# Kernel optimization log

Measured on AMD Instinct MI355X. Metric: run time of the kernel, lower is better.

The kernel has to match this reference:

```python
import jax, jax.numpy as jnp
import numpy as np

N = 25600          # total nodes
B = 64             # graphs in batch
NPG = N // B       # nodes per graph (400)
K = 16             # in-degree (regular graph)
E = N * K          # edges
D = 128            # hidden dim = out dim
L = 4              # DGN layers
NUM_ATOM = 128


def _linear_init(key, out_s, in_s):
    lim = 1.0 / np.sqrt(in_s)
    return jax.random.uniform(key, (out_s, in_s), jnp.float32, -lim, lim)


def setup_inputs() -> dict:
    key = jax.random.key(0)
    ks = jax.random.split(key, 16)
    node_feat = jax.random.randint(ks[0], (N,), 0, NUM_ATOM)
    # K-regular in-degree graph, edges intra-graph; dst sorted
    dst = jnp.repeat(jnp.arange(N), K)                       # [E]
    src_local = jax.random.randint(ks[1], (E,), 0, NPG)
    src = (dst // NPG) * NPG + src_local                     # same graph as dst
    eig = jax.random.normal(ks[2], (E, 2), jnp.float32)
    snorm_n = jnp.full((N, 1), 1.0 / np.sqrt(NPG), jnp.float32)
    graph_ids = jnp.arange(N) // NPG
    emb = jax.random.normal(ks[3], (NUM_ATOM, D), jnp.float32) * 0.02
    pre_W = jnp.stack([_linear_init(jax.random.fold_in(ks[4], i), D, 2 * D) for i in range(L)])
    pre_b = jnp.zeros((L, D), jnp.float32)
    post_W = jnp.stack([_linear_init(jax.random.fold_in(ks[5], i), D, 5 * D) for i in range(L)])
    post_b = jnp.zeros((L, D), jnp.float32)
    r_W0 = _linear_init(ks[6], 64, 128); r_b0 = jnp.zeros((64,), jnp.float32)
    r_W1 = _linear_init(ks[7], 32, 64);  r_b1 = jnp.zeros((32,), jnp.float32)
    r_W2 = _linear_init(ks[8], 128, 32); r_b2 = jnp.zeros((128,), jnp.float32)
    return dict(node_feat=node_feat, src=src, dst=dst, eig=eig, snorm_n=snorm_n,
                graph_ids=graph_ids, emb=emb, pre_W=pre_W, pre_b=pre_b,
                post_W=post_W, post_b=post_b, r_W0=r_W0, r_b0=r_b0,
                r_W1=r_W1, r_b1=r_b1, r_W2=r_W2, r_b2=r_b2)


def _dgn_layer(h, src, dst, eig, snorm_n, Wp, bp, Wq, bq):
    n = h.shape[0]
    # pretrans on edges: Linear(cat(h_src, h_dst))  [E, D]
    z2 = jnp.concatenate([h[src], h[dst]], axis=-1)
    e = jnp.einsum('ei,oi->eo', z2, Wp) + bp
    seg_sum = lambda v: jax.ops.segment_sum(v, dst, num_segments=n, indices_are_sorted=True)
    s = seg_sum(e)
    mean = s / K
    mx = jax.ops.segment_max(e, dst, num_segments=n, indices_are_sorted=True)
    # directional aggregator (eig_idx=1)
    w = eig[:, 1]
    denom = seg_sum(jnp.abs(w)) + 1e-8                       # [n]
    ew = w / denom[dst]                                      # [E]
    dir_agg = jnp.abs(seg_sum(e * ew[:, None]) - seg_sum(ew)[:, None] * h)
    agg = jnp.concatenate([h, mean, s, mx, dir_agg], axis=-1)  # [n, 5D]
    hn = jnp.einsum('ni,oi->no', agg, Wq) + bq
    hn = hn * snorm_n           # graph_norm
    hn = jax.nn.relu(hn)
    return h + hn               # residual (in_dim == out_dim)


def reference(node_feat, src, dst, eig, snorm_n, graph_ids, emb,
              pre_W, pre_b, post_W, post_b,
              r_W0, r_b0, r_W1, r_b1, r_W2, r_b2):
    h = emb[node_feat]                                       # AtomEncoder
    for i in range(L):
        h = _dgn_layer(h, src, dst, eig, snorm_n, pre_W[i], pre_b[i], post_W[i], post_b[i])
    # mean_nodes per graph (equal-sized graphs)
    hg = jax.ops.segment_sum(h, graph_ids, num_segments=B, indices_are_sorted=True) / NPG
    y = jax.nn.relu(hg @ r_W0.T + r_b0)
    y = jax.nn.relu(y @ r_W1.T + r_b1)
    return y @ r_W2.T + r_b2                                 # [B, 128]
```

## Files before the change

### kernel.cpp

```cpp
#include <hip/hip_runtime.h>
#include <cstddef>

#define NN 25600
#define BB 64
#define NPG 400
#define KK 16
#define LL 4

typedef _Float16 half_t;
typedef _Float16 h8 __attribute__((ext_vector_type(8)));
typedef _Float16 h4 __attribute__((ext_vector_type(4)));
typedef _Float16 h2 __attribute__((ext_vector_type(2)));
typedef float f32x4 __attribute__((ext_vector_type(4)));

__global__ __launch_bounds__(256) void prep_k(const float* __restrict__ preW,
                                              const float* __restrict__ preb,
                                              const float* __restrict__ postW,
                                              half_t* __restrict__ WpreH,
                                              half_t* __restrict__ WpreL,
                                              float* __restrict__ bpre,
                                              half_t* __restrict__ WpostH,
                                              half_t* __restrict__ WpostL) {
  int idx = blockIdx.x * 256 + threadIdx.x;
  const int n1 = LL * 256 * 128;
  const int n2 = n1 + LL * 256;
  const int n3 = n2 + LL * 128 * 512;
  if (idx < n1) {
    int l = idx / 32768;
    int q = idx % 32768;
    int j = q & 7, lane = (q >> 3) & 63, kc = (q >> 9) & 3, c16 = q >> 11;
    int col = c16 * 16 + (lane & 15);
    int k = kc * 32 + (lane >> 4) * 8 + j;
    float v = (col < 128) ? preW[(size_t)l * 32768 + (size_t)col * 256 + k]
                          : preW[(size_t)l * 32768 + (size_t)(col - 128) * 256 + 128 + k];
    half_t hi = (half_t)v;
    WpreH[idx] = hi;
    WpreL[idx] = (half_t)(v - (float)hi);
  } else if (idx < n2) {
    int r = idx - n1;
    int l = r / 256, o = r % 256;
    bpre[r] = (o < 128) ? 0.f : preb[l * 128 + (o - 128)];
  } else if (idx < n3) {
    int r = idx - n2;
    int l = r / 65536;
    int q = r % 65536;
    int j = q & 7, lane = (q >> 3) & 63, kc = (q >> 9) & 15, c16 = q >> 13;
    int col = c16 * 16 + (lane & 15);
    int k = kc * 32 + (lane >> 4) * 8 + j;
    int jblk = k >> 7, kk = k & 127;
    const float* base = postW + (size_t)l * 128 * 640 + (size_t)col * 640;
    float v;
    if (jblk == 0)      v = base[kk];
    else if (jblk == 1) v = base[128 + kk] * (1.f / 16.f) + base[256 + kk];
    else if (jblk == 2) v = base[384 + kk];
    else                v = base[512 + kk];
    half_t hi = (half_t)v;
    WpostH[r] = hi;
    WpostL[r] = (half_t)(v - (float)hi);
  }
}

__global__ __launch_bounds__(256) void embed_k(const int* __restrict__ nf,
                                               const float* __restrict__ emb,
                                               half_t* __restrict__ Hh,
                                               half_t* __restrict__ Hl) {
  int idx = blockIdx.x * 256 + threadIdx.x;
  int n = idx >> 5;
  int d4 = idx & 31;
  int a = nf[n];
  float4 v = *(const float4*)(emb + (size_t)a * 128 + d4 * 4);
  h4 hi, lo;
  const float* vp = &v.x;
#pragma unroll
  for (int j = 0; j < 4; ++j) {
    half_t h = (half_t)vp[j];
    hi[j] = h;
    lo[j] = (half_t)(vp[j] - (float)h);
  }
  *(h4*)(Hh + (size_t)n * 128 + d4 * 4) = hi;
  *(h4*)(Hl + (size_t)n * 128 + d4 * 4) = lo;
}

__global__ __launch_bounds__(256) void pre_gemm_k(const half_t* __restrict__ Ah_g,
                                                  const half_t* __restrict__ Al_g,
                                                  const half_t* __restrict__ Wh_g,
                                                  const half_t* __restrict__ Wl_g,
                                                  float* __restrict__ preA) {
  __shared__ half_t Ahs[64][132];
  __shared__ half_t Als[64][132];
  const int tid = threadIdx.x;
  const int bid = blockIdx.x;
  const int swz = (bid & 7) * 50 + (bid >> 3);
  const int r0 = swz * 64;
  const int wid = tid >> 6, lane = tid & 63;
  const int wm = wid >> 1, wn = wid & 1;
  const int lr = lane & 15, lk = (lane >> 4) * 8;
  f32x4 acc[2][4] = {};

  {
    const int row = tid >> 2;
#pragma unroll
    for (int s = 0; s < 4; ++s) {
      const int koff = (tid & 3) * 8 + s * 32;
      const size_t g = (size_t)(r0 + row) * 128 + koff;
      *(h8*)&Ahs[row][koff] = *(const h8*)(Ah_g + g);
      *(h8*)&Als[row][koff] = *(const h8*)(Al_g + g);
    }
  }
  __syncthreads();

#pragma unroll
  for (int kc = 0; kc < 4; ++kc) {
    h8 af[2][2];
#pragma unroll
    for (int mi = 0; mi < 2; ++mi) {
      const int r = wm * 32 + mi * 16 + lr;
      af[mi][0] = *(const h8*)&Ahs[r][kc * 32 + lk];
      af[mi][1] = *(const h8*)&Als[r][kc * 32 + lk];
    }
#pragma unroll
    for (int nj = 0; nj < 4; ++nj) {
      const size_t fi = ((size_t)((wn * 4 + nj) * 4 + kc) * 64 + lane) * 8;
      const h8 b0v = *(const h8*)(Wh_g + fi);
      const h8 b1v = *(const h8*)(Wl_g + fi);
#pragma unroll
      for (int mi = 0; mi < 2; ++mi) {
        acc[mi][nj] = __builtin_amdgcn_mfma_f32_16x16x32_f16(af[mi][0], b0v, acc[mi][nj], 0, 0, 0);
        acc[mi][nj] = __builtin_amdgcn_mfma_f32_16x16x32_f16(af[mi][0], b1v, acc[mi][nj], 0, 0, 0);
        acc[mi][nj] = __builtin_amdgcn_mfma_f32_16x16x32_f16(af[mi][1], b0v, acc[mi][nj], 0, 0, 0);
      }
    }
  }
#pragma unroll
  for (int mi = 0; mi < 2; ++mi) {
    const int rowb = r0 + wm * 32 + mi * 16 + (lane >> 4) * 4;
#pragma unroll
    for (int nj = 0; nj < 4; ++nj) {
      const int col = wn * 64 + nj * 16 + lr;
#pragma unroll
      for (int q = 0; q < 4; ++q) {
        preA[(size_t)(rowb + q) * 128 + col] = acc[mi][nj][q];
      }
    }
  }
}

__global__ __launch_bounds__(256) void agg_post_k(const float* __restrict__ preA,
                                                  const int* __restrict__ src,
                                                  const float* __restrict__ eig,
                                                  const half_t* __restrict__ WpHg,
                                                  const half_t* __restrict__ WpLg,
                                                  const float* __restrict__ bpre128,
                                                  half_t* __restrict__ Hh,
                                                  half_t* __restrict__ Hl,
                                                  const half_t* __restrict__ Wh,
                                                  const half_t* __restrict__ Wl,
                                                  const float* __restrict__ bias,
                                                  const float* __restrict__ snorm) {
  __shared__ half_t Ah[16][392];
  __shared__ half_t Al[16][392];
  __shared__ float bsh[16][132];
  const int tid = threadIdx.x;
  const int bid = blockIdx.x;
  const int swz = (bid & 7) * 200 + (bid >> 3);
  const int r0 = swz * 16;
  const int wid = tid >> 6, lane = tid & 63;
  const int wn = wid;
  const int lr = lane & 15, lk = (lane >> 4) * 8;
  const int d0 = 2 * lane;

  const int frow = r0 + lr;
  h8 afh[4][2];
#pragma unroll
  for (int hc = 0; hc < 4; ++hc) {
    afh[hc][0] = *(const h8*)(Hh + (size_t)frow * 128 + hc * 32 + lk);
    afh[hc][1] = *(const h8*)(Hl + (size_t)frow * 128 + hc * 32 + lk);
  }

  {
    f32x4 bacc[2] = {};
#pragma unroll
    for (int kc = 0; kc < 4; ++kc) {
#pragma unroll
      for (int nj = 0; nj < 2; ++nj) {
        const size_t fi = ((size_t)((8 + wn * 2 + nj) * 4 + kc) * 64 + lane) * 8;
        const h8 b0v = *(const h8*)(WpHg + fi);
        const h8 b1v = *(const h8*)(WpLg + fi);
        bacc[nj] = __builtin_amdgcn_mfma_f32_16x16x32_f16(afh[kc][0], b0v, bacc[nj], 0, 0, 0);
        bacc[nj] = __builtin_amdgcn_mfma_f32_16x16x32_f16(afh[kc][0], b1v, bacc[nj], 0, 0, 0);
        bacc[nj] = __builtin_amdgcn_mfma_f32_16x16x32_f16(afh[kc][1], b0v, bacc[nj], 0, 0, 0);
      }
    }
    const int rowb = (lane >> 4) * 4;
#pragma unroll
    for (int nj = 0; nj < 2; ++nj) {
      const int col = (wn * 2 + nj) * 16 + lr;
      const float bv = bpre128[col];
#pragma unroll
      for (int q = 0; q < 4; ++q) {
        bsh[rowb + q][col] = bacc[nj][q] + bv;
      }
    }
  }
  __syncthreads();

  for (int i = 0; i < 4; ++i) {
    const int lrow = wid * 4 + i;
    const int n = r0 + lrow;
    int sv[KK];
    float wv[KK];
    {
      const int4* sp4 = (const int4*)(src + (size_t)n * KK);
      const float4* ep4 = (const float4*)(eig + (size_t)n * KK * 2);
#pragma unroll
      for (int t = 0; t < 4; ++t) {
        const int4 s4 = sp4[t];
        sv[4 * t + 0] = s4.x;
        sv[4 * t + 1] = s4.y;
        sv[4 * t + 2] = s4.z;
        sv[4 * t + 3] = s4.w;
      }
#pragma unroll
      for (int t = 0; t < 8; ++t) {
        const float4 e4 = ep4[t];
        wv[2 * t + 0] = e4.y;
        wv[2 * t + 1] = e4.w;
      }
    }
    float denom = 0.f;
#pragma unroll
    for (int e = 0; e < KK; ++e) denom += fabsf(wv[e]);
    denom += 1e-8f;
    const float inv = 1.f / denom;
    float sum_ew = 0.f;
#pragma unroll
    for (int e = 0; e < KK; ++e) {
      wv[e] *= inv;
      sum_ew += wv[e];
    }
    float sA0 = 0.f, sA1 = 0.f, wA0 = 0.f, wA1 = 0.f;
    float mA0 = -3.402823466e+38f, mA1 = -3.402823466e+38f;
#pragma unroll
    for (int e = 0; e < KK; ++e) {
      const float2 a = *(const float2*)(preA + (size_t)sv[e] * 128 + d0);
      sA0 += a.x;
      sA1 += a.y;
      wA0 = fmaf(wv[e], a.x, wA0);
      wA1 = fmaf(wv[e], a.y, wA1);
      mA0 = fmaxf(mA0, a.x);
      mA1 = fmaxf(mA1, a.y);
    }
    const float2 b = {bsh[lrow][d0], bsh[lrow][d0 + 1]};
    const h2 hh2 = *(const h2*)(Hh + (size_t)n * 128 + d0);
    const h2 hl2 = *(const h2*)(Hl + (size_t)n * 128 + d0);
    const float hx = (float)hh2[0] + (float)hl2[0];
    const float hy = (float)hh2[1] + (float)hl2[1];
    auto wr2 = [&](int kcol, float v0, float v1) {
      h2 hi, lo;
      hi[0] = (half_t)v0;
      hi[1] = (half_t)v1;
      lo[0] = (half_t)(v0 - (float)hi[0]);
      lo[1] = (half_t)(v1 - (float)hi[1]);
      *(h2*)&Ah[lrow][kcol] = hi;
      *(h2*)&Al[lrow][kcol] = lo;
    };
    wr2(d0, sA0 + 16.f * b.x, sA1 + 16.f * b.y);
    wr2(128 + d0, mA0 + b.x, mA1 + b.y);
    wr2(256 + d0, fabsf(wA0 + sum_ew * (b.x - hx)), fabsf(wA1 + sum_ew * (b.y - hy)));
  }
  __syncthreads();

  f32x4 acc[2] = {};
#pragma unroll
  for (int kc = 0; kc < 16; ++kc) {
    h8 a0, a1;
    if (kc < 4) {
      a0 = afh[kc & 3][0];
      a1 = afh[kc & 3][1];
    } else {
      a0 = *(const h8*)&Ah[lr][(kc - 4) * 32 + lk];
      a1 = *(const h8*)&Al[lr][(kc - 4) * 32 + lk];
    }
#pragma unroll
    for (int nj = 0; nj < 2; ++nj) {
      const size_t fi = ((size_t)((wn * 2 + nj) * 16 + kc) * 64 + lane) * 8;
      const h8 b0v = *(const h8*)(Wh + fi);
      const h8 b1v = *(const h8*)(Wl + fi);
      acc[nj] = __builtin_amdgcn_mfma_f32_16x16x32_f16(a0, b0v, acc[nj], 0, 0, 0);
      acc[nj] = __builtin_amdgcn_mfma_f32_16x16x32_f16(a0, b1v, acc[nj], 0, 0, 0);
      acc[nj] = __builtin_amdgcn_mfma_f32_16x16x32_f16(a1, b0v, acc[nj], 0, 0, 0);
    }
  }

  const int rowb = r0 + (lane >> 4) * 4;
#pragma unroll
  for (int nj = 0; nj < 2; ++nj) {
    const int col = wn * 32 + nj * 16 + lr;
    const float bv = bias[col];
#pragma unroll
    for (int q = 0; q < 4; ++q) {
      const int r = rowb + q;
      float a = acc[nj][q] + bv;
      a *= snorm[r];
      a = fmaxf(a, 0.f);
      const size_t off = (size_t)r * 128 + col;
      const float hold = (float)Hh[off] + (float)Hl[off];
      const float hn = hold + a;
      const half_t hi = (half_t)hn;
      Hh[off] = hi;
      Hl[off] = (half_t)(hn - (float)hi);
    }
  }
}

__global__ __launch_bounds__(256) void reduce_mlp_k(const half_t* __restrict__ Hh,
                                                    const half_t* __restrict__ Hl,
                                                    const float* __restrict__ W0, const float* __restrict__ b0,
                                                    const float* __restrict__ W1, const float* __restrict__ b1,
                                                    const float* __restrict__ W2, const float* __restrict__ b2,
                                                    float* __restrict__ out) {
  __shared__ float hgs[128];
  __shared__ float red[128];
  __shared__ float y0s[64];
  __shared__ float y1s[32];
  __shared__ float wb[64 * 130];
  const int g = blockIdx.x;
  const int t = threadIdx.x;
  {
    const int d = t & 127, hf = t >> 7;
    const size_t base = ((size_t)g * NPG + (size_t)hf * 200) * 128 + d;
    float acc = 0.f;
    for (int i = 0; i < 200; ++i) {
      const size_t off = base + (size_t)i * 128;
      acc += (float)Hh[off] + (float)Hl[off];
    }
    if (hf) red[d] = acc;
    __syncthreads();
    if (!hf) hgs[d] = (acc + red[d]) * (1.f / (float)NPG);
  }
  __syncthreads();
  for (int idx = t; idx < 64 * 128; idx += 256) {
    wb[(idx >> 7) * 130 + (idx & 127)] = W0[idx];
  }
  __syncthreads();
  if (t < 64) {
    float a = b0[t];
    const float* w = &wb[t * 130];
    for (int k = 0; k < 128; ++k) a = fmaf(hgs[k], w[k], a);
    y0s[t] = fmaxf(a, 0.f);
  }
  __syncthreads();
  for (int idx = t; idx < 32 * 64; idx += 256) {
    wb[(idx >> 6) * 66 + (idx & 63)] = W1[idx];
  }
  __syncthreads();
  if (t < 32) {
    float a = b1[t];
    const float* w = &wb[t * 66];
    for (int k = 0; k < 64; ++k) a = fmaf(y0s[k], w[k], a);
    y1s[t] = fmaxf(a, 0.f);
  }
  __syncthreads();
  for (int idx = t; idx < 128 * 32; idx += 256) {
    wb[(idx >> 5) * 34 + (idx & 31)] = W2[idx];
  }
  __syncthreads();
  if (t < 128) {
    float a = b2[t];
    const float* w = &wb[t * 34];
    for (int k = 0; k < 32; ++k) a = fmaf(y1s[k], w[k], a);
    out[(size_t)g * 128 + t] = a;
  }
}

extern "C" void kernel_launch(void* const* d_in, const int* in_sizes, int n_in,
                              void* d_out, int out_size, void* d_ws, size_t ws_size,
                              hipStream_t stream) {
  const int* node_feat = (const int*)d_in[0];
  const int* src = (const int*)d_in[1];
  const float* eig = (const float*)d_in[3];
  const float* snorm = (const float*)d_in[4];
  const float* emb = (const float*)d_in[6];
  const float* preW = (const float*)d_in[7];
  const float* preb = (const float*)d_in[8];
  const float* postW = (const float*)d_in[9];
  const float* postb = (const float*)d_in[10];
  const float* rW0 = (const float*)d_in[11];
  const float* rb0 = (const float*)d_in[12];
  const float* rW1 = (const float*)d_in[13];
  const float* rb1 = (const float*)d_in[14];
  const float* rW2 = (const float*)d_in[15];
  const float* rb2 = (const float*)d_in[16];
  float* out = (float*)d_out;

  half_t* Hh = (half_t*)d_ws;
  half_t* Hl = Hh + (size_t)NN * 128;
  float* preA = (float*)(Hl + (size_t)NN * 128);
  half_t* WpreH = (half_t*)(preA + (size_t)NN * 128);
  half_t* WpreL = WpreH + (size_t)LL * 32768;
  half_t* WpostH = WpreL + (size_t)LL * 32768;
  half_t* WpostL = WpostH + (size_t)LL * 65536;
  float* bpre = (float*)(WpostL + (size_t)LL * 65536);

  prep_k<<<1540, 256, 0, stream>>>(preW, preb, postW, WpreH, WpreL, bpre, WpostH, WpostL);
  embed_k<<<(NN * 32) / 256, 256, 0, stream>>>(node_feat, emb, Hh, Hl);

  for (int l = 0; l < LL; ++l) {
    pre_gemm_k<<<NN / 64, 256, 0, stream>>>(
        Hh, Hl, WpreH + (size_t)l * 32768, WpreL + (size_t)l * 32768, preA);
    agg_post_k<<<NN / 16, 256, 0, stream>>>(
        preA, src, eig,
        WpreH + (size_t)l * 32768, WpreL + (size_t)l * 32768,
        bpre + (size_t)l * 256 + 128,
        Hh, Hl,
        WpostH + (size_t)l * 65536, WpostL + (size_t)l * 65536,
        postb + (size_t)l * 128, snorm);
  }

  reduce_mlp_k<<<BB, 256, 0, stream>>>(Hh, Hl, rW0, rb0, rW1, rb1, rW2, rb2, out);
}
```

Before: 280.1 us.

## Double the aggregation kernel's wave count and stage neighbor gathers through LDS via async loads

The aggregation/post-GEMM kernel now launches 512 threads (8 waves) per 16-row block, each wave owning one 16-column slice of the MFMA work and two node rows of aggregation instead of four. Neighbor feature rows of preA are brought in with global_load_lds into a per-wave LDS staging buffer, split into 8-edge chunks and interleaved with index/weight loads and reductions behind explicit waitcnt barriers. The aim is more memory-level parallelism and latency hiding for the random gather. In exchange LDS use grows by 32KB per block, which may limit occupancy, and the hand-placed waitcnts are fragile.

```diff
diff --git a/kernel.cpp b/kernel.cpp
--- a/kernel.cpp
+++ b/kernel.cpp
@@ -12,6 +12,9 @@
 typedef _Float16 h4 __attribute__((ext_vector_type(4)));
 typedef _Float16 h2 __attribute__((ext_vector_type(2)));
 typedef float f32x4 __attribute__((ext_vector_type(4)));
+
+#define GCAST(p) ((const __attribute__((address_space(1))) void*)(p))
+#define SCAST(p) ((__attribute__((address_space(3))) void*)(p))
 
 __global__ __launch_bounds__(256) void prep_k(const float* __restrict__ preW,
                                               const float* __restrict__ preb,
@@ -145,21 +148,22 @@
   }
 }
 
-__global__ __launch_bounds__(256) void agg_post_k(const float* __restrict__ preA,
-                                                  const int* __restrict__ src,
-                                                  const float* __restrict__ eig,
-                                                  const half_t* __restrict__ WpHg,
-                                                  const half_t* __restrict__ WpLg,
-                                                  const float* __restrict__ bpre128,
-                                                  half_t* __restrict__ Hh,
-                                                  half_t* __restrict__ Hl,
-                                                  const half_t* __restrict__ Wh,
-                                                  const half_t* __restrict__ Wl,
-                                                  const float* __restrict__ bias,
-                                                  const float* __restrict__ snorm) {
+__global__ __launch_bounds__(512, 4) void agg_post_k(const float* __restrict__ preA,
+                                                     const int* __restrict__ src,
+                                                     const float* __restrict__ eig,
+                                                     const half_t* __restrict__ WpHg,
+                                                     const half_t* __restrict__ WpLg,
+                                                     const float* __restrict__ bpre128,
+                                                     half_t* __restrict__ Hh,
+                                                     half_t* __restrict__ Hl,
+                                                     const half_t* __restrict__ Wh,
+                                                     const half_t* __restrict__ Wl,
+                                                     const float* __restrict__ bias,
+                                                     const float* __restrict__ snorm) {
   __shared__ half_t Ah[16][392];
   __shared__ half_t Al[16][392];
   __shared__ float bsh[16][132];
+  __shared__ float stage[8][8][128];
   const int tid = threadIdx.x;
   const int bid = blockIdx.x;
   const int swz = (bid & 7) * 200 + (bid >> 3);
@@ -168,6 +172,85 @@
   const int wn = wid;
   const int lr = lane & 15, lk = (lane >> 4) * 8;
   const int d0 = 2 * lane;
+  const int glane = (lane & 31) * 4;
+  const int gsel = lane >> 5;
+
+#define LOAD_SE(sv, wv, n)                                              \
+  {                                                                     \
+    const int4* sp4 = (const int4*)(src + (size_t)(n) * KK);            \
+    const float4* ep4 = (const float4*)(eig + (size_t)(n) * KK * 2);    \
+    _Pragma("unroll")                                                   \
+    for (int t = 0; t < 4; ++t) {                                       \
+      const int4 s4 = sp4[t];                                           \
+      sv[4 * t + 0] = s4.x; sv[4 * t + 1] = s4.y;                       \
+      sv[4 * t + 2] = s4.z; sv[4 * t + 3] = s4.w;                       \
+    }                                                                   \
+    _Pragma("unroll")                                                   \
+    for (int t = 0; t < 8; ++t) {                                       \
+      const float4 e4 = ep4[t];                                         \
+      wv[2 * t + 0] = e4.y; wv[2 * t + 1] = e4.w;                       \
+    }                                                                   \
+  }
+#define ISSUE_CHUNK(sv, base)                                                        \
+  {                                                                                  \
+    _Pragma("unroll")                                                                \
+    for (int c = 0; c < 4; ++c) {                                                    \
+      const float* gp = preA + (size_t)sv[(base) + 2 * c + gsel] * 128 + glane;      \
+      __builtin_amdgcn_global_load_lds(GCAST(gp), SCAST(&stage[wid][2 * c][0]),      \
+                                       16, 0, 0);                                    \
+    }                                                                                \
+  }
+#define CONSUME_CHUNK(wv, base, sX, sY, wX, wY, mX, mY)                              \
+  {                                                                                  \
+    _Pragma("unroll")                                                                \
+    for (int e = 0; e < 8; ++e) {                                                    \
+      const float2 a = *(const float2*)&stage[wid][e][d0];                           \
+      const float w = wv[(base) + e];                                                \
+      sX += a.x; sY += a.y;                                                          \
+      wX = fmaf(w, a.x, wX); wY = fmaf(w, a.y, wY);                                  \
+      mX = fmaxf(mX, a.x); mY = fmaxf(mY, a.y);                                      \
+    }                                                                                \
+  }
+#define WEIGHTS(wv, inv, sum_ew)                                                     \
+  {                                                                                  \
+    float denom = 0.f;                                                               \
+    _Pragma("unroll")                                                                \
+    for (int e = 0; e < KK; ++e) denom += fabsf(wv[e]);                              \
+    denom += 1e-8f;                                                                  \
+    inv = 1.f / denom;                                                               \
+    sum_ew = 0.f;                                                                    \
+    _Pragma("unroll")                                                                \
+    for (int e = 0; e < KK; ++e) { wv[e] *= inv; sum_ew += wv[e]; }                  \
+  }
+#define WRITE_ROW(lrow, n, sX, sY, wX, wY, mX, mY, sum_ew)                           \
+  {                                                                                  \
+    const float2 b = {bsh[lrow][d0], bsh[lrow][d0 + 1]};                             \
+    const h2 hh2 = *(const h2*)(Hh + (size_t)(n) * 128 + d0);                        \
+    const h2 hl2 = *(const h2*)(Hl + (size_t)(n) * 128 + d0);                        \
+    const float hx = (float)hh2[0] + (float)hl2[0];                                  \
+    const float hy = (float)hh2[1] + (float)hl2[1];                                  \
+    auto wr2 = [&](int kcol, float v0, float v1) {                                   \
+      h2 hi, lo;                                                                     \
+      hi[0] = (half_t)v0; hi[1] = (half_t)v1;                                        \
+      lo[0] = (half_t)(v0 - (float)hi[0]);                                           \
+      lo[1] = (half_t)(v1 - (float)hi[1]);                                           \
+      *(h2*)&Ah[lrow][kcol] = hi;                                                    \
+      *(h2*)&Al[lrow][kcol] = lo;                                                    \
+    };                                                                               \
+    wr2(d0, sX + 16.f * b.x, sY + 16.f * b.y);                                       \
+    wr2(128 + d0, mX + b.x, mY + b.y);                                               \
+    wr2(256 + d0, fabsf(wX + sum_ew * (b.x - hx)),                                   \
+                  fabsf(wY + sum_ew * (b.y - hy)));                                  \
+  }
+#define LGKM0 asm volatile("s_waitcnt lgkmcnt(0)" ::: "memory");
+#define VM0   asm volatile("s_waitcnt vmcnt(0)" ::: "memory");
+
+  const int lrowA = wid * 2;
+  const int nA = r0 + lrowA;
+  int svA[KK];
+  float wvA[KK];
+  LOAD_SE(svA, wvA, nA)
+  ISSUE_CHUNK(svA, 0)
 
   const int frow = r0 + lr;
   h8 afh[4][2];
@@ -178,99 +261,59 @@
   }
 
   {
-    f32x4 bacc[2] = {};
+    f32x4 bacc = {};
 #pragma unroll
     for (int kc = 0; kc < 4; ++kc) {
-#pragma unroll
-      for (int nj = 0; nj < 2; ++nj) {
-        const size_t fi = ((size_t)((8 + wn * 2 + nj) * 4 + kc) * 64 + lane) * 8;
-        const h8 b0v = *(const h8*)(WpHg + fi);
-        const h8 b1v = *(const h8*)(WpLg + fi);
-        bacc[nj] = __builtin_amdgcn_mfma_f32_16x16x32_f16(afh[kc][0], b0v, bacc[nj], 0, 0, 0);
-        bacc[nj] = __builtin_amdgcn_mfma_f32_16x16x32_f16(afh[kc][0], b1v, bacc[nj], 0, 0, 0);
-        bacc[nj] = __builtin_amdgcn_mfma_f32_16x16x32_f16(afh[kc][1], b0v, bacc[nj], 0, 0, 0);
-      }
+      const size_t fi = ((size_t)((8 + wn) * 4 + kc) * 64 + lane) * 8;
+      const h8 b0v = *(const h8*)(WpHg + fi);
+      const h8 b1v = *(const h8*)(WpLg + fi);
+      bacc = __builtin_amdgcn_mfma_f32_16x16x32_f16(afh[kc][0], b0v, bacc, 0, 0, 0);
+      bacc = __builtin_amdgcn_mfma_f32_16x16x32_f16(afh[kc][0], b1v, bacc, 0, 0, 0);
+      bacc = __builtin_amdgcn_mfma_f32_16x16x32_f16(afh[kc][1], b0v, bacc, 0, 0, 0);
     }
     const int rowb = (lane >> 4) * 4;
-#pragma unroll
-    for (int nj = 0; nj < 2; ++nj) {
-      const int col = (wn * 2 + nj) * 16 + lr;
-      const float bv = bpre128[col];
-#pragma unroll
-      for (int q = 0; q < 4; ++q) {
-        bsh[rowb + q][col] = bacc[nj][q] + bv;
-      }
-    }
-  }
-  __syncthreads();
-
-  for (int i = 0; i < 4; ++i) {
-    const int lrow = wid * 4 + i;
-    const int n = r0 + lrow;
-    int sv[KK];
-    float wv[KK];
-    {
-      const int4* sp4 = (const int4*)(src + (size_t)n * KK);
-      const float4* ep4 = (const float4*)(eig + (size_t)n * KK * 2);
-#pragma unroll
-      for (int t = 0; t < 4; ++t) {
-        const int4 s4 = sp4[t];
-        sv[4 * t + 0] = s4.x;
-        sv[4 * t + 1] = s4.y;
-        sv[4 * t + 2] = s4.z;
-        sv[4 * t + 3] = s4.w;
-      }
-#pragma unroll
-      for (int t = 0; t < 8; ++t) {
-        const float4 e4 = ep4[t];
-        wv[2 * t + 0] = e4.y;
-        wv[2 * t + 1] = e4.w;
-      }
-    }
-    float denom = 0.f;
-#pragma unroll
-    for (int e = 0; e < KK; ++e) denom += fabsf(wv[e]);
-    denom += 1e-8f;
-    const float inv = 1.f / denom;
-    float sum_ew = 0.f;
-#pragma unroll
-    for (int e = 0; e < KK; ++e) {
-      wv[e] *= inv;
-      sum_ew += wv[e];
-    }
-    float sA0 = 0.f, sA1 = 0.f, wA0 = 0.f, wA1 = 0.f;
-    float mA0 = -3.402823466e+38f, mA1 = -3.402823466e+38f;
-#pragma unroll
-    for (int e = 0; e < KK; ++e) {
-      const float2 a = *(const float2*)(preA + (size_t)sv[e] * 128 + d0);
-      sA0 += a.x;
-      sA1 += a.y;
-      wA0 = fmaf(wv[e], a.x, wA0);
-      wA1 = fmaf(wv[e], a.y, wA1);
-      mA0 = fmaxf(mA0, a.x);
-      mA1 = fmaxf(mA1, a.y);
-    }
-    const float2 b = {bsh[lrow][d0], bsh[lrow][d0 + 1]};
-    const h2 hh2 = *(const h2*)(Hh + (size_t)n * 128 + d0);
-    const h2 hl2 = *(const h2*)(Hl + (size_t)n * 128 + d0);
-    const float hx = (float)hh2[0] + (float)hl2[0];
-    const float hy = (float)hh2[1] + (float)hl2[1];
-    auto wr2 = [&](int kcol, float v0, float v1) {
-      h2 hi, lo;
-      hi[0] = (half_t)v0;
-      hi[1] = (half_t)v1;
-      lo[0] = (half_t)(v0 - (float)hi[0]);
-      lo[1] = (half_t)(v1 - (float)hi[1]);
-      *(h2*)&Ah[lrow][kcol] = hi;
-      *(h2*)&Al[lrow][kcol] = lo;
-    };
-    wr2(d0, sA0 + 16.f * b.x, sA1 + 16.f * b.y);
-    wr2(128 + d0, mA0 + b.x, mA1 + b.y);
-    wr2(256 + d0, fabsf(wA0 + sum_ew * (b.x - hx)), fabsf(wA1 + sum_ew * (b.y - hy)));
-  }
-  __syncthreads();
-
-  f32x4 acc[2] = {};
+    const int col = wn * 16 + lr;
+    const float bv = bpre128[col];
+#pragma unroll
+    for (int q = 0; q < 4; ++q) {
+      bsh[rowb + q][col] = bacc[q] + bv;
+    }
+  }
+  __syncthreads();
+
+  {
+    float invA, sewA;
+    WEIGHTS(wvA, invA, sewA)
+    float sX = 0.f, sY = 0.f, wX = 0.f, wY = 0.f;
+    float mX = -3.402823466e+38f, mY = -3.402823466e+38f;
+    CONSUME_CHUNK(wvA, 0, sX, sY, wX, wY, mX, mY)
+    LGKM0
+    ISSUE_CHUNK(svA, 8)
+    const int lrowB = lrowA + 1;
+    const int nB = nA + 1;
+    int svB[KK];
+    float wvB[KK];
+    LOAD_SE(svB, wvB, nB)
+    float invB, sewB;
+    WEIGHTS(wvB, invB, sewB)
+    VM0
+    CONSUME_CHUNK(wvA, 8, sX, sY, wX, wY, mX, mY)
+    WRITE_ROW(lrowA, nA, sX, sY, wX, wY, mX, mY, sewA)
+    LGKM0
+    ISSUE_CHUNK(svB, 0)
+    float sX2 = 0.f, sY2 = 0.f, wX2 = 0.f, wY2 = 0.f;
+    float mX2 = -3.402823466e+38f, mY2 = -3.402823466e+38f;
+    VM0
+    CONSUME_CHUNK(wvB, 0, sX2, sY2, wX2, wY2, mX2, mY2)
+    LGKM0
+    ISSUE_CHUNK(svB, 8)
+    VM0
+    CONSUME_CHUNK(wvB, 8, sX2, sY2, wX2, wY2, mX2, mY2)
+    WRITE_ROW(lrowB, nB, sX2, sY2, wX2, wY2, mX2, mY2, sewB)
+  }
+  __syncthreads();
+
+  f32x4 acc = {};
 #pragma unroll
   for (int kc = 0; kc < 16; ++kc) {
     h8 a0, a1;
@@ -281,26 +324,22 @@
       a0 = *(const h8*)&Ah[lr][(kc - 4) * 32 + lk];
       a1 = *(const h8*)&Al[lr][(kc - 4) * 32 + lk];
     }
-#pragma unroll
-    for (int nj = 0; nj < 2; ++nj) {
-      const size_t fi = ((size_t)((wn * 2 + nj) * 16 + kc) * 64 + lane) * 8;
-      const h8 b0v = *(const h8*)(Wh + fi);
-      const h8 b1v = *(const h8*)(Wl + fi);
-      acc[nj] = __builtin_amdgcn_mfma_f32_16x16x32_f16(a0, b0v, acc[nj], 0, 0, 0);
-      acc[nj] = __builtin_amdgcn_mfma_f32_16x16x32_f16(a0, b1v, acc[nj], 0, 0, 0);
-      acc[nj] = __builtin_amdgcn_mfma_f32_16x16x32_f16(a1, b0v, acc[nj], 0, 0, 0);
-    }
-  }
-
-  const int rowb = r0 + (lane >> 4) * 4;
-#pragma unroll
-  for (int nj = 0; nj < 2; ++nj) {
-    const int col = wn * 32 + nj * 16 + lr;
+    const size_t fi = ((size_t)(wn * 16 + kc) * 64 + lane) * 8;
+    const h8 b0v = *(const h8*)(Wh + fi);
+    const h8 b1v = *(const h8*)(Wl + fi);
+    acc = __builtin_amdgcn_mfma_f32_16x16x32_f16(a0, b0v, acc, 0, 0, 0);
+    acc = __builtin_amdgcn_mfma_f32_16x16x32_f16(a0, b1v, acc, 0, 0, 0);
+    acc = __builtin_amdgcn_mfma_f32_16x16x32_f16(a1, b0v, acc, 0, 0, 0);
+  }
+
+  {
+    const int rowb = r0 + (lane >> 4) * 4;
+    const int col = wn * 16 + lr;
     const float bv = bias[col];
 #pragma unroll
     for (int q = 0; q < 4; ++q) {
       const int r = rowb + q;
-      float a = acc[nj][q] + bv;
+      float a = acc[q] + bv;
       a *= snorm[r];
       a = fmaxf(a, 0.f);
       const size_t off = (size_t)r * 128 + col;
@@ -311,6 +350,13 @@
       Hl[off] = (half_t)(hn - (float)hi);
     }
   }
+#undef LOAD_SE
+#undef ISSUE_CHUNK
+#undef CONSUME_CHUNK
+#undef WEIGHTS
+#undef WRITE_ROW
+#undef LGKM0
+#undef VM0
 }
 
 __global__ __launch_bounds__(256) void reduce_mlp_k(const half_t* __restrict__ Hh,
@@ -408,7 +454,7 @@
   for (int l = 0; l < LL; ++l) {
     pre_gemm_k<<<NN / 64, 256, 0, stream>>>(
         Hh, Hl, WpreH + (size_t)l * 32768, WpreL + (size_t)l * 32768, preA);
-    agg_post_k<<<NN / 16, 256, 0, stream>>>(
+    agg_post_k<<<NN / 16, 512, 0, stream>>>(
         preA, src, eig,
         WpreH + (size_t)l * 32768, WpreL + (size_t)l * 32768,
         bpre + (size_t)l * 256 + 128,
```

Result: no change. 278.5 us (-0.6%).
